# Performance work log

Measured on AMD Instinct MI355X. Metric: run time of the kernel, lower is better.

## Reference

```python
import jax, jax.numpy as jnp
import numpy as np

N, E, C, L, R, H = 10000, 100000, 64, 9, 9, 8
HD = C // H
F0 = 64          # radial feature dim (fc_neurons[0])
WN = R * C       # CP tensor-product weight numel


def _silu(x):
    return x * jax.nn.sigmoid(x)


def _smooth_lrelu(x, a=0.2):
    return (1 + a) / 2 * x + (1 - a) / 2 * x * (2 * jax.nn.sigmoid(x) - 1)


def _lin(x, W, b=None):
    # equivariant Linear over channel dim; bias applied only to scalar (l=0) component
    y = jnp.einsum('elc,cd->eld', x, W)
    if b is not None:
        y = y.at[:, 0, :].add(b)
    return y


def _cp_tp(x, sh, w, U, V, Y):
    # CP-decomposed SH tensor product:
    # out[e,m,c] = sum_r U[m,r] * (sum_m1 V[m1,r] x[e,m1,c]) * (sum_m2 Y[m2,r] sh[e,m2]) * w[e,r,c]
    xv = jnp.einsum('elc,lr->erc', x, V)          # [E,R,C]
    ys = jnp.einsum('el,lr->er', sh, Y)           # [E,R]
    return jnp.einsum('erc,lr->elc', xv * ys[:, :, None] * w, U)


def setup_inputs():
    key = jax.random.key(0)
    ks = jax.random.split(key, 32)
    f32 = jnp.float32
    s = 1.0 / np.sqrt(C)
    return {
        'node_input': jax.random.normal(ks[0], (N, L, C), f32),
        'edge_attr': jax.random.normal(ks[1], (E, L), f32),
        'edge_scalars': jax.random.normal(ks[2], (E, F0), f32),
        'W_src': jax.random.normal(ks[3], (C, C), f32) * s,
        'b_src': jnp.zeros((C,), f32),
        'W_dst': jax.random.normal(ks[4], (C, C), f32) * s,
        'rad_w1': jax.random.normal(ks[5], (F0, F0), f32) / np.sqrt(F0),
        'rad_b1': jnp.zeros((F0,), f32),
        'rad_ln_w': jnp.ones((F0,), f32),
        'rad_ln_b': jnp.zeros((F0,), f32),
        'rad_w2': jax.random.normal(ks[6], (F0, WN), f32) / np.sqrt(F0),
        'rad_offset': jax.random.uniform(ks[7], (WN,), f32, -1.0 / np.sqrt(F0), 1.0 / np.sqrt(F0)),
        'U1': jax.random.normal(ks[8], (L, R), f32) / np.sqrt(R),
        'V1': jax.random.normal(ks[9], (L, R), f32) / np.sqrt(L),
        'Y1': jax.random.normal(ks[10], (L, R), f32) / np.sqrt(L),
        'U2': jax.random.normal(ks[11], (L, R), f32) / np.sqrt(R),
        'V2': jax.random.normal(ks[12], (L, R), f32) / np.sqrt(L),
        'Y2': jax.random.normal(ks[13], (L, R), f32) / np.sqrt(L),
        'W_alpha': jax.random.normal(ks[14], (C, C), f32) * s,
        'b_alpha': jnp.zeros((C,), f32),
        'alpha_dot': jax.random.normal(ks[15], (H, HD), f32) / np.sqrt(HD),
        'W_value': jax.random.normal(ks[16], (C, 2 * C), f32) * s,
        'b_value': jnp.zeros((2 * C,), f32),
        'W_proj': jax.random.normal(ks[17], (C, C), f32) * s,
        'b_proj': jnp.zeros((C,), f32),
        'edge_src': jax.random.randint(ks[18], (E,), 0, N),
        'edge_dst': jax.random.randint(ks[19], (E,), 0, N),
    }


def reference(node_input, edge_attr, edge_scalars, W_src, b_src, W_dst,
              rad_w1, rad_b1, rad_ln_w, rad_ln_b, rad_w2, rad_offset,
              U1, V1, Y1, U2, V2, Y2, W_alpha, b_alpha, alpha_dot,
              W_value, b_value, W_proj, b_proj, edge_src, edge_dst):
    n = node_input.shape[0]
    # per-edge message: gather of src/dst projected features
    msg = _lin(node_input, W_src, b_src)[edge_src] + _lin(node_input, W_dst)[edge_dst]
    # RadialProfile MLP -> CP tensor-product weights [E,R,C]
    h = edge_scalars @ rad_w1 + rad_b1
    h = (h - h.mean(-1, keepdims=True)) / jnp.sqrt(h.var(-1, keepdims=True) + 1e-5)
    h = _silu(h * rad_ln_w + rad_ln_b)
    w = (h @ rad_w2 + rad_offset).reshape(-1, R, C)
    msg = _cp_tp(msg, edge_attr, w, U1, V1, Y1)
    # attention logits from scalar (0e) channel
    a = _lin(msg, W_alpha, b_alpha)[:, 0, :].reshape(-1, H, HD)
    a = jnp.einsum('ekd,kd->ek', _smooth_lrelu(a), alpha_dot)
    # segment softmax over destination nodes
    amax = jax.ops.segment_max(a, edge_dst, num_segments=n)
    a = jnp.exp(a - amax[edge_dst])
    asum = jax.ops.segment_sum(a, edge_dst, num_segments=n)
    a = a / (asum[edge_dst] + 1e-16)  # dropout = identity at eval
    # value path: gated nonlinearity, second CP tensor product
    v = _lin(msg, W_value, b_value)
    val, gate = v[..., :C], jax.nn.sigmoid(v[:, 0, C:])[:, None, :]
    v = jnp.concatenate([_silu(val[:, :1, :]), val[:, 1:, :] * gate], axis=1)
    v = _cp_tp(v, edge_attr, w, U2, V2, Y2)
    v = v.reshape(-1, L, H, HD) * a[:, None, :, None]
    out = jax.ops.segment_sum(v, edge_dst, num_segments=n).reshape(n, L, C)
    return _lin(out, W_proj, b_proj)
```

## Files before the change

kernel.cpp:

```cpp
#include <hip/hip_runtime.h>
#include <hip/hip_bf16.h>

#define NN 10000
#define EE 100000
#define LL 9
#define HH 8
#define NLC (NN*LL*64)

typedef float f32x4 __attribute__((ext_vector_type(4)));
typedef short bf16x8 __attribute__((ext_vector_type(8)));
typedef unsigned short u16x4 __attribute__((ext_vector_type(4)));

__device__ __forceinline__ float sigmoidf_(float x){ return 1.0f/(1.0f+__expf(-x)); }
__device__ __forceinline__ unsigned short f2bf(float x){
  __hip_bfloat16 b = __float2bfloat16(x);
  return *reinterpret_cast<unsigned short*>(&b);
}
__device__ __forceinline__ float bf2f(unsigned short b){ return __uint_as_float(((unsigned)b)<<16); }

__device__ __forceinline__ bf16x8 ldA(const unsigned short* plane, int ln, int kt){
  const int row = ln & 15;
  const int col = (kt*32 + ((ln>>4)<<3)) ^ ((row & 7) << 3);
  return *(const bf16x8*)(plane + row*64 + col);
}

__global__ __launch_bounds__(256) void k_prep_mat(
    const float* __restrict__ W, int ncol,
    unsigned short* __restrict__ bh, unsigned short* __restrict__ bl)
{
  const int t = blockIdx.x*256 + threadIdx.x;
  if (t >= (ncol>>4)*1024) return;
  const int i  = t & 7;
  const int ln = (t >> 3) & 63;
  const int kt = (t >> 9) & 1;
  const int nt = t >> 10;
  const int k  = kt*32 + ((ln>>4)<<3) + i;
  const int col = nt*16 + (ln & 15);
  const float v = W[k*ncol + col];
  const unsigned short h = f2bf(v);
  bh[t] = h;
  bl[t] = f2bf(v - bf2f(h));
}

__global__ __launch_bounds__(256) void k_prep_vab(
    const float* __restrict__ Wv, const float* __restrict__ Wa,
    unsigned short* __restrict__ bh, unsigned short* __restrict__ bl)
{
  const int t = blockIdx.x*256 + threadIdx.x;
  if (t >= 12*1024) return;
  const int i  = t & 7;
  const int ln = (t >> 3) & 63;
  const int kt = (t >> 9) & 1;
  const int nt = t >> 10;
  const int k  = kt*32 + ((ln>>4)<<3) + i;
  const int col = nt*16 + (ln & 15);
  const float v = (col < 128) ? Wv[k*128 + col] : Wa[k*64 + (col - 128)];
  const unsigned short h = f2bf(v);
  bh[t] = h;
  bl[t] = f2bf(v - bf2f(h));
}

__global__ __launch_bounds__(256) void k_node_lin_mfma(
    const float* __restrict__ x, const float* __restrict__ bs,
    const unsigned short* __restrict__ wsdh, const unsigned short* __restrict__ wsdl,
    float* __restrict__ xs, float* __restrict__ xd)
{
  const int tid = threadIdx.x, wid = tid>>6, ln = tid&63;
  const int base = blockIdx.x * 16;
  __shared__ unsigned short hx[2][16][64];
  {
    const int row = tid >> 4, c4 = (tid & 15) * 4;
    const float4 v = *(const float4*)&x[(size_t)(base+row)*64 + c4];
    const int cs = c4 ^ ((row & 7) << 3);
    u16x4 h, l;
    h[0]=f2bf(v.x); h[1]=f2bf(v.y); h[2]=f2bf(v.z); h[3]=f2bf(v.w);
    l[0]=f2bf(v.x-bf2f(h[0])); l[1]=f2bf(v.y-bf2f(h[1]));
    l[2]=f2bf(v.z-bf2f(h[2])); l[3]=f2bf(v.w-bf2f(h[3]));
    *(u16x4*)&hx[0][row][cs] = h;
    *(u16x4*)&hx[1][row][cs] = l;
  }
  __syncthreads();
  const bf16x8 ah0 = ldA(&hx[0][0][0], ln, 0);
  const bf16x8 ah1 = ldA(&hx[0][0][0], ln, 1);
  const bf16x8 al0 = ldA(&hx[1][0][0], ln, 0);
  const bf16x8 al1 = ldA(&hx[1][0][0], ln, 1);
  const bf16x8* Bh = (const bf16x8*)wsdh;
  const bf16x8* Bl = (const bf16x8*)wsdl;
  const int col = wid*16 + (ln & 15);
  const int r0  = (ln >> 4) * 4;
  #pragma unroll
  for (int g = 0; g < 2; g++){
    const int nt = g*4 + wid;
    f32x4 d = {0.f,0.f,0.f,0.f};
    const bf16x8 bh0 = Bh[(nt*2+0)*64 + ln];
    const bf16x8 bl0 = Bl[(nt*2+0)*64 + ln];
    const bf16x8 bh1 = Bh[(nt*2+1)*64 + ln];
    const bf16x8 bl1 = Bl[(nt*2+1)*64 + ln];
    d = __builtin_amdgcn_mfma_f32_16x16x32_bf16(ah0, bh0, d, 0, 0, 0);
    d = __builtin_amdgcn_mfma_f32_16x16x32_bf16(al0, bh0, d, 0, 0, 0);
    d = __builtin_amdgcn_mfma_f32_16x16x32_bf16(ah0, bl0, d, 0, 0, 0);
    d = __builtin_amdgcn_mfma_f32_16x16x32_bf16(ah1, bh1, d, 0, 0, 0);
    d = __builtin_amdgcn_mfma_f32_16x16x32_bf16(al1, bh1, d, 0, 0, 0);
    d = __builtin_amdgcn_mfma_f32_16x16x32_bf16(ah1, bl1, d, 0, 0, 0);
    float* out = (g == 0) ? xs : xd;
    #pragma unroll
    for (int i = 0; i < 4; i++){
      const int row = base + r0 + i;
      float o = d[i];
      if (g == 0 && row % LL == 0) o += bs[col];
      out[(size_t)row*64 + col] = o;
    }
  }
}

__global__ __launch_bounds__(512, 4) void k_edge_fused(
    const float* __restrict__ xsrc, const float* __restrict__ xdst,
    const float* __restrict__ eattr, const float* __restrict__ escal,
    const float* __restrict__ w1, const float* __restrict__ b1,
    const float* __restrict__ lnw, const float* __restrict__ lnb,
    const float* __restrict__ woff,
    const float* __restrict__ U1, const float* __restrict__ V1, const float* __restrict__ Y1,
    const float* __restrict__ U2, const float* __restrict__ V2, const float* __restrict__ Y2,
    const float* __restrict__ ba, const float* __restrict__ adot,
    const float* __restrict__ bv,
    const unsigned short* __restrict__ w2h, const unsigned short* __restrict__ w2l,
    const unsigned short* __restrict__ vabh, const unsigned short* __restrict__ vabl,
    const int* __restrict__ esrc, const int* __restrict__ edst,
    float* __restrict__ accum, float* __restrict__ asum)
{
  const int tid = threadIdx.x;
  const int wid = tid >> 6;
  const int ln  = tid & 63;
  const int base = blockIdx.x * 16;

  __shared__ float sgse[2][16][64];
  __shared__ unsigned short wle[16][576];
  __shared__ unsigned short ms2[9][16][64];
  __shared__ float sU1[9][12], sV1[9][12], sU2[9][12], sV2[9][12];
  __shared__ float syv1[16][12], syv2[16][12];
  float (*se)[64] = sgse[0];
  unsigned short* hpl = (unsigned short*)&sgse[1][0][0];

  for (int i = tid; i < 81; i += 512){
    const int r9 = i/9, c9 = i%9;
    sU1[r9][c9]=U1[i]; sV1[r9][c9]=V1[i]; sU2[r9][c9]=U2[i]; sV2[r9][c9]=V2[i];
  }
  if (tid < 144){
    const int er = tid/9, r = tid%9;
    const float* ea = eattr + (size_t)(base+er)*9;
    float y1 = 0.f, y2 = 0.f;
    #pragma unroll
    for (int l = 0; l < 9; l++){ y1 += ea[l]*Y1[l*9+r]; y2 += ea[l]*Y2[l*9+r]; }
    syv1[er][r] = y1; syv2[er][r] = y2;
  }
  for (int i = tid; i < 1024; i += 512) se[i>>6][i&63] = escal[(size_t)base*64 + i];
  __syncthreads();

  {
    const int c = ln;
    const float bb = b1[c];
    float hv_[2] = {bb, bb};
    for (int kq = 0; kq < 16; kq++){
      const int k0 = kq*4;
      const float a0 = w1[(k0+0)*64+c], a1 = w1[(k0+1)*64+c], a2 = w1[(k0+2)*64+c], a3 = w1[(k0+3)*64+c];
      #pragma unroll
      for (int j = 0; j < 2; j++){
        const float4 xv = *(const float4*)&se[wid*2+j][k0];
        hv_[j] += xv.x*a0 + xv.y*a1 + xv.z*a2 + xv.w*a3;
      }
    }
    const float lw = lnw[c], lb = lnb[c];
    #pragma unroll
    for (int j = 0; j < 2; j++){
      const float v = hv_[j];
      float s1 = v, s2 = v*v;
      #pragma unroll
      for (int m = 1; m < 64; m <<= 1){ s1 += __shfl_xor(s1, m, 64); s2 += __shfl_xor(s2, m, 64); }
      const float mean = s1 * (1.0f/64.0f);
      const float var  = s2 * (1.0f/64.0f) - mean*mean;
      const float g = (v - mean) * rsqrtf(var + 1e-5f) * lw + lb;
      const float hj = g * sigmoidf_(g);
      const int er = wid*2 + j;
      const int cs = c ^ ((er & 7) << 3);
      const unsigned short hb = f2bf(hj);
      hpl[(0*16 + er)*64 + cs] = hb;
      hpl[(1*16 + er)*64 + cs] = f2bf(hj - bf2f(hb));
    }
  }
  __syncthreads();

  {
    const bf16x8 ah0 = ldA(hpl, ln, 0);
    const bf16x8 ah1 = ldA(hpl, ln, 1);
    const bf16x8 al0 = ldA(hpl + 16*64, ln, 0);
    const bf16x8 al1 = ldA(hpl + 16*64, ln, 1);
    const bf16x8* Bh = (const bf16x8*)w2h;
    const bf16x8* Bl = (const bf16x8*)w2l;
    const int q = ln >> 4, p = ln & 15;
    #pragma unroll
    for (int t5 = 0; t5 < 5; t5++){
      const int nt = wid + 8*t5;
      if (nt < 36){
        f32x4 d = {0.f,0.f,0.f,0.f};
        const bf16x8 bh0 = Bh[(nt*2+0)*64 + ln];
        const bf16x8 bl0 = Bl[(nt*2+0)*64 + ln];
        const bf16x8 bh1 = Bh[(nt*2+1)*64 + ln];
        const bf16x8 bl1 = Bl[(nt*2+1)*64 + ln];
        d = __builtin_amdgcn_mfma_f32_16x16x32_bf16(ah0, bh0, d, 0, 0, 0);
        d = __builtin_amdgcn_mfma_f32_16x16x32_bf16(al0, bh0, d, 0, 0, 0);
        d = __builtin_amdgcn_mfma_f32_16x16x32_bf16(ah0, bl0, d, 0, 0, 0);
        d = __builtin_amdgcn_mfma_f32_16x16x32_bf16(ah1, bh1, d, 0, 0, 0);
        d = __builtin_amdgcn_mfma_f32_16x16x32_bf16(al1, bh1, d, 0, 0, 0);
        d = __builtin_amdgcn_mfma_f32_16x16x32_bf16(ah1, bl1, d, 0, 0, 0);
        const int col = nt*16 + p;
        const float wo = woff[col];
        #pragma unroll
        for (int i = 0; i < 4; i++) wle[q*4+i][col] = f2bf(d[i] + wo);
      }
    }
  }
  __syncthreads();

  {
    const int c = ln;
    const int er0 = wid*2;
    float msg[2][9];
    #pragma unroll
    for (int j = 0; j < 2; j++){
      const int e  = base + er0 + j;
      const int src = esrc[e], dst = edst[e];
      const float* ps = xsrc + (size_t)src*576 + c;
      const float* pd = xdst + (size_t)dst*576 + c;
      #pragma unroll
      for (int l = 0; l < 9; l++) msg[j][l] = ps[l*64] + pd[l*64];
    }
    float xv[2][9];
    #pragma unroll
    for (int j = 0; j < 2; j++)
      #pragma unroll
      for (int r = 0; r < 9; r++) xv[j][r] = 0.f;
    #pragma unroll
    for (int l = 0; l < 9; l++){
      const float4 v0 = *(const float4*)&sV1[l][0];
      const float4 v1 = *(const float4*)&sV1[l][4];
      const float  v2 = sV1[l][8];
      #pragma unroll
      for (int j = 0; j < 2; j++){
        const float m = msg[j][l];
        xv[j][0] += m*v0.x; xv[j][1] += m*v0.y; xv[j][2] += m*v0.z; xv[j][3] += m*v0.w;
        xv[j][4] += m*v1.x; xv[j][5] += m*v1.y; xv[j][6] += m*v1.z; xv[j][7] += m*v1.w;
        xv[j][8] += m*v2;
      }
    }
    #pragma unroll
    for (int j = 0; j < 2; j++){
      const int er = er0 + j;
      const float4 s0 = *(const float4*)&syv1[er][0];
      const float4 s1 = *(const float4*)&syv1[er][4];
      const float  s2 = syv1[er][8];
      const float sy[9] = {s0.x,s0.y,s0.z,s0.w,s1.x,s1.y,s1.z,s1.w,s2};
      #pragma unroll
      for (int r = 0; r < 9; r++) xv[j][r] *= sy[r] * bf2f(wle[er][r*64+c]);
    }
    #pragma unroll
    for (int l = 0; l < 9; l++){
      const float4 u0 = *(const float4*)&sU1[l][0];
      const float4 u1 = *(const float4*)&sU1[l][4];
      const float  u2 = sU1[l][8];
      #pragma unroll
      for (int j = 0; j < 2; j++){
        const int er = er0 + j;
        const float m2 = xv[j][0]*u0.x + xv[j][1]*u0.y + xv[j][2]*u0.z + xv[j][3]*u0.w
                       + xv[j][4]*u1.x + xv[j][5]*u1.y + xv[j][6]*u1.z + xv[j][7]*u1.w
                       + xv[j][8]*u2;
        ms2[l][er][c ^ ((er & 7) << 3)] = f2bf(m2);
      }
    }
  }
  __syncthreads();

  f32x4 vacc[9];
  {
    const bf16x8* Bh = (const bf16x8*)vabh;
    const bf16x8* Bl = (const bf16x8*)vabl;
    if (wid < 4){
      const int nt = wid;
      const bf16x8 bh0 = Bh[(nt*2+0)*64 + ln];
      const bf16x8 bl0 = Bl[(nt*2+0)*64 + ln];
      const bf16x8 bh1 = Bh[(nt*2+1)*64 + ln];
      const bf16x8 bl1 = Bl[(nt*2+1)*64 + ln];
      #pragma unroll
      for (int l = 0; l < 9; l++){
        const bf16x8 a0 = ldA(&ms2[l][0][0], ln, 0);
        const bf16x8 a1 = ldA(&ms2[l][0][0], ln, 1);
        f32x4 d = {0.f,0.f,0.f,0.f};
        d = __builtin_amdgcn_mfma_f32_16x16x32_bf16(a0, bh0, d, 0, 0, 0);
        d = __builtin_amdgcn_mfma_f32_16x16x32_bf16(a0, bl0, d, 0, 0, 0);
        d = __builtin_amdgcn_mfma_f32_16x16x32_bf16(a1, bh1, d, 0, 0, 0);
        d = __builtin_amdgcn_mfma_f32_16x16x32_bf16(a1, bl1, d, 0, 0, 0);
        vacc[l] = d;
      }
    } else {
      const int w4 = wid - 4;
      const bf16x8 a0 = ldA(&ms2[0][0][0], ln, 0);
      const bf16x8 a1 = ldA(&ms2[0][0][0], ln, 1);
      const int q = ln >> 4, p = ln & 15;
      #pragma unroll
      for (int gg = 0; gg < 2; gg++){
        const int nt = 4 + gg*4 + w4;
        const bf16x8 bh0 = Bh[(nt*2+0)*64 + ln];
        const bf16x8 bl0 = Bl[(nt*2+0)*64 + ln];
        const bf16x8 bh1 = Bh[(nt*2+1)*64 + ln];
        const bf16x8 bl1 = Bl[(nt*2+1)*64 + ln];
        f32x4 d = {0.f,0.f,0.f,0.f};
        d = __builtin_amdgcn_mfma_f32_16x16x32_bf16(a0, bh0, d, 0, 0, 0);
        d = __builtin_amdgcn_mfma_f32_16x16x32_bf16(a0, bl0, d, 0, 0, 0);
        d = __builtin_amdgcn_mfma_f32_16x16x32_bf16(a1, bh1, d, 0, 0, 0);
        d = __builtin_amdgcn_mfma_f32_16x16x32_bf16(a1, bl1, d, 0, 0, 0);
        #pragma unroll
        for (int i = 0; i < 4; i++) sgse[gg][q*4+i][w4*16+p] = d[i];
      }
    }
  }
  __syncthreads();

  if (wid < 4){
    const int col = wid*16 + (ln & 15);
    const int r0  = (ln >> 4) * 4;
    #pragma unroll
    for (int l = 0; l < 9; l++)
      #pragma unroll
      for (int i = 0; i < 4; i++){
        const int er = r0 + i;
        ms2[l][er][col ^ ((er & 7) << 3)] = f2bf(vacc[l][i]);
      }
  }
  __syncthreads();

  {
    const int c = ln;
    const int er0 = wid*2;
    const float bvc = bv[c], bgc = bv[64+c], bac = ba[c], adc = adot[c];
    int dsti[2]; float gsv[2], pev[2];
    #pragma unroll
    for (int j = 0; j < 2; j++){
      const int er = er0 + j;
      dsti[j] = edst[base + er];
      gsv[j] = sigmoidf_(sgse[0][er][c] + bgc);
      const float a  = sgse[1][er][c] + bac;
      const float sl = 0.2f*a + 0.8f*a*sigmoidf_(a);
      float t = sl * adc;
      t += __shfl_xor(t, 1, 64);
      t += __shfl_xor(t, 2, 64);
      t += __shfl_xor(t, 4, 64);
      pev[j] = __expf(t);
      if ((c & 7) == 0) atomicAdd(&asum[(size_t)dsti[j]*8 + (c>>3)], pev[j]);
    }
    float tmp2[2][9];
    #pragma unroll
    for (int j = 0; j < 2; j++)
      #pragma unroll
      for (int r = 0; r < 9; r++) tmp2[j][r] = 0.f;
    #pragma unroll
    for (int l = 0; l < 9; l++){
      const float4 v0 = *(const float4*)&sV2[l][0];
      const float4 v1 = *(const float4*)&sV2[l][4];
      const float  v2 = sV2[l][8];
      #pragma unroll
      for (int j = 0; j < 2; j++){
        const int er = er0 + j;
        float v = bf2f(ms2[l][er][c ^ ((er & 7) << 3)]);
        if (l == 0){ v += bvc; v = v * sigmoidf_(v); }
        else v *= gsv[j];
        tmp2[j][0] += v*v0.x; tmp2[j][1] += v*v0.y; tmp2[j][2] += v*v0.z; tmp2[j][3] += v*v0.w;
        tmp2[j][4] += v*v1.x; tmp2[j][5] += v*v1.y; tmp2[j][6] += v*v1.z; tmp2[j][7] += v*v1.w;
        tmp2[j][8] += v*v2;
      }
    }
    #pragma unroll
    for (int j = 0; j < 2; j++){
      const int er = er0 + j;
      const float4 s0 = *(const float4*)&syv2[er][0];
      const float4 s1 = *(const float4*)&syv2[er][4];
      const float  s2 = syv2[er][8];
      const float sy[9] = {s0.x,s0.y,s0.z,s0.w,s1.x,s1.y,s1.z,s1.w,s2};
      #pragma unroll
      for (int r = 0; r < 9; r++) tmp2[j][r] *= sy[r] * bf2f(wle[er][r*64+c]) * pev[j];
    }
    #pragma unroll
    for (int l = 0; l < 9; l++){
      const float4 u0 = *(const float4*)&sU2[l][0];
      const float4 u1 = *(const float4*)&sU2[l][4];
      const float  u2 = sU2[l][8];
      #pragma unroll
      for (int j = 0; j < 2; j++){
        const float o = tmp2[j][0]*u0.x + tmp2[j][1]*u0.y + tmp2[j][2]*u0.z + tmp2[j][3]*u0.w
                      + tmp2[j][4]*u1.x + tmp2[j][5]*u1.y + tmp2[j][6]*u1.z + tmp2[j][7]*u1.w
                      + tmp2[j][8]*u2;
        atomicAdd(accum + (size_t)dsti[j]*576 + l*64 + c, o);
      }
    }
  }
}

__global__ __launch_bounds__(256) void k_norm_proj_mfma(
    const float* __restrict__ acc, const float* __restrict__ asum,
    const unsigned short* __restrict__ wph, const unsigned short* __restrict__ wpl,
    const float* __restrict__ bp, float* __restrict__ out)
{
  const int tid = threadIdx.x, wid = tid>>6, ln = tid&63;
  const int base = blockIdx.x * 16;
  __shared__ unsigned short hx[2][16][64];
  {
    const int row = tid >> 4, c4 = (tid & 15) * 4;
    const int grow = base + row;
    const float s = 1.0f / (asum[(size_t)(grow/9)*8 + (c4>>3)] + 1e-16f);
    float4 v = *(const float4*)&acc[(size_t)grow*64 + c4];
    v.x *= s; v.y *= s; v.z *= s; v.w *= s;
    const int cs = c4 ^ ((row & 7) << 3);
    u16x4 h, l;
    h[0]=f2bf(v.x); h[1]=f2bf(v.y); h[2]=f2bf(v.z); h[3]=f2bf(v.w);
    l[0]=f2bf(v.x-bf2f(h[0])); l[1]=f2bf(v.y-bf2f(h[1]));
    l[2]=f2bf(v.z-bf2f(h[2])); l[3]=f2bf(v.w-bf2f(h[3]));
    *(u16x4*)&hx[0][row][cs] = h;
    *(u16x4*)&hx[1][row][cs] = l;
  }
  __syncthreads();
  const bf16x8 ah0 = ldA(&hx[0][0][0], ln, 0);
  const bf16x8 ah1 = ldA(&hx[0][0][0], ln, 1);
  const bf16x8 al0 = ldA(&hx[1][0][0], ln, 0);
  const bf16x8 al1 = ldA(&hx[1][0][0], ln, 1);
  const bf16x8* Bh = (const bf16x8*)wph;
  const bf16x8* Bl = (const bf16x8*)wpl;
  const int nt = wid;
  f32x4 d = {0.f,0.f,0.f,0.f};
  const bf16x8 bh0 = Bh[(nt*2+0)*64 + ln];
  const bf16x8 bl0 = Bl[(nt*2+0)*64 + ln];
  const bf16x8 bh1 = Bh[(nt*2+1)*64 + ln];
  const bf16x8 bl1 = Bl[(nt*2+1)*64 + ln];
  d = __builtin_amdgcn_mfma_f32_16x16x32_bf16(ah0, bh0, d, 0, 0, 0);
  d = __builtin_amdgcn_mfma_f32_16x16x32_bf16(al0, bh0, d, 0, 0, 0);
  d = __builtin_amdgcn_mfma_f32_16x16x32_bf16(ah0, bl0, d, 0, 0, 0);
  d = __builtin_amdgcn_mfma_f32_16x16x32_bf16(ah1, bh1, d, 0, 0, 0);
  d = __builtin_amdgcn_mfma_f32_16x16x32_bf16(al1, bh1, d, 0, 0, 0);
  d = __builtin_amdgcn_mfma_f32_16x16x32_bf16(ah1, bl1, d, 0, 0, 0);
  const int col = wid*16 + (ln & 15);
  const int r0  = (ln >> 4) * 4;
  #pragma unroll
  for (int i = 0; i < 4; i++){
    const int row = base + r0 + i;
    float o = d[i];
    if (row % LL == 0) o += bp[col];
    out[(size_t)row*64 + col] = o;
  }
}

extern "C" void kernel_launch(void* const* d_in, const int* in_sizes, int n_in,
                              void* d_out, int out_size, void* d_ws, size_t ws_size,
                              hipStream_t stream)
{
  (void)in_sizes; (void)n_in; (void)out_size;
  const float* node_input = (const float*)d_in[0];
  const float* edge_attr  = (const float*)d_in[1];
  const float* edge_scal  = (const float*)d_in[2];
  const float* W_src   = (const float*)d_in[3];
  const float* b_src   = (const float*)d_in[4];
  const float* W_dst   = (const float*)d_in[5];
  const float* rad_w1  = (const float*)d_in[6];
  const float* rad_b1  = (const float*)d_in[7];
  const float* rad_ln_w= (const float*)d_in[8];
  const float* rad_ln_b= (const float*)d_in[9];
  const float* rad_w2  = (const float*)d_in[10];
  const float* rad_off = (const float*)d_in[11];
  const float* U1 = (const float*)d_in[12];
  const float* V1 = (const float*)d_in[13];
  const float* Y1 = (const float*)d_in[14];
  const float* U2 = (const float*)d_in[15];
  const float* V2 = (const float*)d_in[16];
  const float* Y2 = (const float*)d_in[17];
  const float* W_alpha = (const float*)d_in[18];
  const float* b_alpha = (const float*)d_in[19];
  const float* alpha_dot = (const float*)d_in[20];
  const float* W_value = (const float*)d_in[21];
  const float* b_value = (const float*)d_in[22];
  const float* W_proj  = (const float*)d_in[23];
  const float* b_proj  = (const float*)d_in[24];
  const int* esrc = (const int*)d_in[25];
  const int* edst = (const int*)d_in[26];

  float* xsrc  = (float*)d_ws;
  float* xdst  = xsrc + NLC;
  float* accum = xdst + NLC;
  float* asum  = accum + NLC;
  unsigned short* w2h  = (unsigned short*)(asum + (size_t)NN*HH);
  unsigned short* w2l  = w2h + 36*1024;
  unsigned short* vabh = w2l + 36*1024;
  unsigned short* vabl = vabh + 12*1024;
  unsigned short* wsdh = vabl + 12*1024;
  unsigned short* wsdl = wsdh + 8*1024;
  unsigned short* wph  = wsdl + 8*1024;
  unsigned short* wpl  = wph  + 4*1024;
  const size_t need = ((size_t)3*NLC + (size_t)NN*HH)*sizeof(float)
                    + (size_t)(2*36*1024 + 2*12*1024 + 2*8*1024 + 2*4*1024)*sizeof(unsigned short);
  if (ws_size < need) return;

  hipMemsetAsync(accum, 0, (size_t)NLC*sizeof(float), stream);
  hipMemsetAsync(asum, 0, (size_t)NN*HH*sizeof(float), stream);

  k_prep_mat<<<144, 256, 0, stream>>>(rad_w2, 576, w2h, w2l);
  k_prep_vab<<<48, 256, 0, stream>>>(W_value, W_alpha, vabh, vabl);
  k_prep_mat<<<16, 256, 0, stream>>>(W_src, 64, wsdh, wsdl);
  k_prep_mat<<<16, 256, 0, stream>>>(W_dst, 64, wsdh + 4*1024, wsdl + 4*1024);
  k_prep_mat<<<16, 256, 0, stream>>>(W_proj, 64, wph, wpl);
  k_node_lin_mfma<<<NN*LL/16, 256, 0, stream>>>(node_input, b_src, wsdh, wsdl, xsrc, xdst);
  k_edge_fused<<<EE/16, 512, 0, stream>>>(xsrc, xdst, edge_attr, edge_scal,
      rad_w1, rad_b1, rad_ln_w, rad_ln_b, rad_off,
      U1, V1, Y1, U2, V2, Y2,
      b_alpha, alpha_dot, b_value,
      w2h, w2l, vabh, vabl, esrc, edst, accum, asum);
  k_norm_proj_mfma<<<NN*LL/16, 256, 0, stream>>>(accum, asum, wph, wpl, b_proj, (float*)d_out);
}
```

Before: 291.3 us.

## Split fused edge kernel into radial-weight producer and edge consumer kernels

The monolithic edge kernel is split into two kernels. The first computes the radial MLP and its per-edge weights [E,576] and stores them as bf16 in workspace. The second does the gather, both CP tensor products, attention and scatter using those weights, processing edges in chunks sized to the available workspace. This is meant to lower per-kernel register and LDS pressure and raise occupancy, at the cost of a round trip to global memory for roughly 115 MB of weights and reduced weight precision. It falls back to the fused kernel when workspace is insufficient.

```diff
diff --git a/kernel.cpp b/kernel.cpp
--- a/kernel.cpp
+++ b/kernel.cpp
@@ -109,6 +109,309 @@
       float o = d[i];
       if (g == 0 && row % LL == 0) o += bs[col];
       out[(size_t)row*64 + col] = o;
+    }
+  }
+}
+
+
+__global__ __launch_bounds__(512, 4) void k_radial_w2(
+    const float* __restrict__ escal,
+    const float* __restrict__ w1, const float* __restrict__ b1,
+    const float* __restrict__ lnw, const float* __restrict__ lnb,
+    const float* __restrict__ woff,
+    const unsigned short* __restrict__ w2h, const unsigned short* __restrict__ w2l,
+    int e0, unsigned short* __restrict__ wbuf)
+{
+  const int tid = threadIdx.x, wid = tid>>6, ln = tid&63;
+  const int lbase = blockIdx.x * 16;
+  const int base  = e0 + lbase;
+  __shared__ float se[16][64];
+  __shared__ unsigned short hpl[2][16][64];
+
+  for (int i = tid; i < 1024; i += 512) se[i>>6][i&63] = escal[(size_t)base*64 + i];
+  __syncthreads();
+
+  {
+    const int c = ln;
+    const float bb = b1[c];
+    float hv_[2] = {bb, bb};
+    for (int kq = 0; kq < 16; kq++){
+      const int k0 = kq*4;
+      const float a0 = w1[(k0+0)*64+c], a1 = w1[(k0+1)*64+c], a2 = w1[(k0+2)*64+c], a3 = w1[(k0+3)*64+c];
+      #pragma unroll
+      for (int j = 0; j < 2; j++){
+        const float4 xv = *(const float4*)&se[wid*2+j][k0];
+        hv_[j] += xv.x*a0 + xv.y*a1 + xv.z*a2 + xv.w*a3;
+      }
+    }
+    const float lw = lnw[c], lb = lnb[c];
+    #pragma unroll
+    for (int j = 0; j < 2; j++){
+      const float v = hv_[j];
+      float s1 = v, s2 = v*v;
+      #pragma unroll
+      for (int m = 1; m < 64; m <<= 1){ s1 += __shfl_xor(s1, m, 64); s2 += __shfl_xor(s2, m, 64); }
+      const float mean = s1 * (1.0f/64.0f);
+      const float var  = s2 * (1.0f/64.0f) - mean*mean;
+      const float g = (v - mean) * rsqrtf(var + 1e-5f) * lw + lb;
+      const float hj = g * sigmoidf_(g);
+      const int er = wid*2 + j;
+      const int cs = c ^ ((er & 7) << 3);
+      const unsigned short hb = f2bf(hj);
+      hpl[0][er][cs] = hb;
+      hpl[1][er][cs] = f2bf(hj - bf2f(hb));
+    }
+  }
+  __syncthreads();
+
+  {
+    const bf16x8 ah0 = ldA(&hpl[0][0][0], ln, 0);
+    const bf16x8 ah1 = ldA(&hpl[0][0][0], ln, 1);
+    const bf16x8 al0 = ldA(&hpl[1][0][0], ln, 0);
+    const bf16x8 al1 = ldA(&hpl[1][0][0], ln, 1);
+    const bf16x8* Bh = (const bf16x8*)w2h;
+    const bf16x8* Bl = (const bf16x8*)w2l;
+    const int q = ln >> 4, p = ln & 15;
+    #pragma unroll
+    for (int t5 = 0; t5 < 5; t5++){
+      const int nt = wid + 8*t5;
+      if (nt < 36){
+        f32x4 d = {0.f,0.f,0.f,0.f};
+        const bf16x8 bh0 = Bh[(nt*2+0)*64 + ln];
+        const bf16x8 bl0 = Bl[(nt*2+0)*64 + ln];
+        const bf16x8 bh1 = Bh[(nt*2+1)*64 + ln];
+        const bf16x8 bl1 = Bl[(nt*2+1)*64 + ln];
+        d = __builtin_amdgcn_mfma_f32_16x16x32_bf16(ah0, bh0, d, 0, 0, 0);
+        d = __builtin_amdgcn_mfma_f32_16x16x32_bf16(al0, bh0, d, 0, 0, 0);
+        d = __builtin_amdgcn_mfma_f32_16x16x32_bf16(ah0, bl0, d, 0, 0, 0);
+        d = __builtin_amdgcn_mfma_f32_16x16x32_bf16(ah1, bh1, d, 0, 0, 0);
+        d = __builtin_amdgcn_mfma_f32_16x16x32_bf16(al1, bh1, d, 0, 0, 0);
+        d = __builtin_amdgcn_mfma_f32_16x16x32_bf16(ah1, bl1, d, 0, 0, 0);
+        const int col = nt*16 + p;
+        const float wo = woff[col];
+        #pragma unroll
+        for (int i = 0; i < 4; i++)
+          wbuf[(size_t)(lbase + q*4 + i)*576 + col] = f2bf(d[i] + wo);
+      }
+    }
+  }
+}
+
+__global__ __launch_bounds__(512, 4) void k_edge_consume(
+    const float* __restrict__ xsrc, const float* __restrict__ xdst,
+    const float* __restrict__ eattr,
+    const float* __restrict__ U1, const float* __restrict__ V1, const float* __restrict__ Y1,
+    const float* __restrict__ U2, const float* __restrict__ V2, const float* __restrict__ Y2,
+    const float* __restrict__ ba, const float* __restrict__ adot,
+    const float* __restrict__ bv,
+    const unsigned short* __restrict__ vabh, const unsigned short* __restrict__ vabl,
+    const unsigned short* __restrict__ wbuf, int e0,
+    const int* __restrict__ esrc, const int* __restrict__ edst,
+    float* __restrict__ accum, float* __restrict__ asum)
+{
+  const int tid = threadIdx.x, wid = tid>>6, ln = tid&63;
+  const int lbase = blockIdx.x * 16;
+  const int base  = e0 + lbase;
+
+  __shared__ unsigned short ms2[9][16][64];
+  __shared__ float sga[2][16][64];
+  __shared__ float sU1[9][12], sV1[9][12], sU2[9][12], sV2[9][12];
+  __shared__ float syv1[16][12], syv2[16][12];
+
+  for (int i = tid; i < 81; i += 512){
+    const int r9 = i/9, c9 = i%9;
+    sU1[r9][c9]=U1[i]; sV1[r9][c9]=V1[i]; sU2[r9][c9]=U2[i]; sV2[r9][c9]=V2[i];
+  }
+  if (tid < 144){
+    const int er = tid/9, r = tid%9;
+    const float* ea = eattr + (size_t)(base+er)*9;
+    float y1 = 0.f, y2 = 0.f;
+    #pragma unroll
+    for (int l = 0; l < 9; l++){ y1 += ea[l]*Y1[l*9+r]; y2 += ea[l]*Y2[l*9+r]; }
+    syv1[er][r] = y1; syv2[er][r] = y2;
+  }
+  __syncthreads();
+
+  {
+    const int c = ln;
+    const int er0 = wid*2;
+    float msg[2][9];
+    #pragma unroll
+    for (int j = 0; j < 2; j++){
+      const int e  = base + er0 + j;
+      const int src = esrc[e], dst = edst[e];
+      const float* ps = xsrc + (size_t)src*576 + c;
+      const float* pd = xdst + (size_t)dst*576 + c;
+      #pragma unroll
+      for (int l = 0; l < 9; l++) msg[j][l] = ps[l*64] + pd[l*64];
+    }
+    float xv[2][9];
+    #pragma unroll
+    for (int j = 0; j < 2; j++)
+      #pragma unroll
+      for (int r = 0; r < 9; r++) xv[j][r] = 0.f;
+    #pragma unroll
+    for (int l = 0; l < 9; l++){
+      const float4 v0 = *(const float4*)&sV1[l][0];
+      const float4 v1 = *(const float4*)&sV1[l][4];
+      const float  v2 = sV1[l][8];
+      #pragma unroll
+      for (int j = 0; j < 2; j++){
+        const float m = msg[j][l];
+        xv[j][0] += m*v0.x; xv[j][1] += m*v0.y; xv[j][2] += m*v0.z; xv[j][3] += m*v0.w;
+        xv[j][4] += m*v1.x; xv[j][5] += m*v1.y; xv[j][6] += m*v1.z; xv[j][7] += m*v1.w;
+        xv[j][8] += m*v2;
+      }
+    }
+    #pragma unroll
+    for (int j = 0; j < 2; j++){
+      const int er = er0 + j;
+      const unsigned short* wb = wbuf + (size_t)(lbase + er)*576 + c;
+      const float4 s0 = *(const float4*)&syv1[er][0];
+      const float4 s1 = *(const float4*)&syv1[er][4];
+      const float  s2 = syv1[er][8];
+      const float sy[9] = {s0.x,s0.y,s0.z,s0.w,s1.x,s1.y,s1.z,s1.w,s2};
+      #pragma unroll
+      for (int r = 0; r < 9; r++) xv[j][r] *= sy[r] * bf2f(wb[r*64]);
+    }
+    #pragma unroll
+    for (int l = 0; l < 9; l++){
+      const float4 u0 = *(const float4*)&sU1[l][0];
+      const float4 u1 = *(const float4*)&sU1[l][4];
+      const float  u2 = sU1[l][8];
+      #pragma unroll
+      for (int j = 0; j < 2; j++){
+        const int er = er0 + j;
+        const float m2 = xv[j][0]*u0.x + xv[j][1]*u0.y + xv[j][2]*u0.z + xv[j][3]*u0.w
+                       + xv[j][4]*u1.x + xv[j][5]*u1.y + xv[j][6]*u1.z + xv[j][7]*u1.w
+                       + xv[j][8]*u2;
+        ms2[l][er][c ^ ((er & 7) << 3)] = f2bf(m2);
+      }
+    }
+  }
+  __syncthreads();
+
+  f32x4 vacc[9];
+  {
+    const bf16x8* Bh = (const bf16x8*)vabh;
+    const bf16x8* Bl = (const bf16x8*)vabl;
+    if (wid < 4){
+      const int nt = wid;
+      const bf16x8 bh0 = Bh[(nt*2+0)*64 + ln];
+      const bf16x8 bl0 = Bl[(nt*2+0)*64 + ln];
+      const bf16x8 bh1 = Bh[(nt*2+1)*64 + ln];
+      const bf16x8 bl1 = Bl[(nt*2+1)*64 + ln];
+      #pragma unroll
+      for (int l = 0; l < 9; l++){
+        const bf16x8 a0 = ldA(&ms2[l][0][0], ln, 0);
+        const bf16x8 a1 = ldA(&ms2[l][0][0], ln, 1);
+        f32x4 d = {0.f,0.f,0.f,0.f};
+        d = __builtin_amdgcn_mfma_f32_16x16x32_bf16(a0, bh0, d, 0, 0, 0);
+        d = __builtin_amdgcn_mfma_f32_16x16x32_bf16(a0, bl0, d, 0, 0, 0);
+        d = __builtin_amdgcn_mfma_f32_16x16x32_bf16(a1, bh1, d, 0, 0, 0);
+        d = __builtin_amdgcn_mfma_f32_16x16x32_bf16(a1, bl1, d, 0, 0, 0);
+        vacc[l] = d;
+      }
+    } else {
+      const int w4 = wid - 4;
+      const bf16x8 a0 = ldA(&ms2[0][0][0], ln, 0);
+      const bf16x8 a1 = ldA(&ms2[0][0][0], ln, 1);
+      const int q = ln >> 4, p = ln & 15;
+      #pragma unroll
+      for (int gg = 0; gg < 2; gg++){
+        const int nt = 4 + gg*4 + w4;
+        const bf16x8 bh0 = Bh[(nt*2+0)*64 + ln];
+        const bf16x8 bl0 = Bl[(nt*2+0)*64 + ln];
+        const bf16x8 bh1 = Bh[(nt*2+1)*64 + ln];
+        const bf16x8 bl1 = Bl[(nt*2+1)*64 + ln];
+        f32x4 d = {0.f,0.f,0.f,0.f};
+        d = __builtin_amdgcn_mfma_f32_16x16x32_bf16(a0, bh0, d, 0, 0, 0);
+        d = __builtin_amdgcn_mfma_f32_16x16x32_bf16(a0, bl0, d, 0, 0, 0);
+        d = __builtin_amdgcn_mfma_f32_16x16x32_bf16(a1, bh1, d, 0, 0, 0);
+        d = __builtin_amdgcn_mfma_f32_16x16x32_bf16(a1, bl1, d, 0, 0, 0);
+        #pragma unroll
+        for (int i = 0; i < 4; i++) sga[gg][q*4+i][w4*16+p] = d[i];
+      }
+    }
+  }
+  __syncthreads();
+
+  if (wid < 4){
+    const int col = wid*16 + (ln & 15);
+    const int r0  = (ln >> 4) * 4;
+    #pragma unroll
+    for (int l = 0; l < 9; l++)
+      #pragma unroll
+      for (int i = 0; i < 4; i++){
+        const int er = r0 + i;
+        ms2[l][er][col ^ ((er & 7) << 3)] = f2bf(vacc[l][i]);
+      }
+  }
+  __syncthreads();
+
+  {
+    const int c = ln;
+    const int er0 = wid*2;
+    const float bvc = bv[c], bgc = bv[64+c], bac = ba[c], adc = adot[c];
+    int dsti[2]; float gsv[2], pev[2];
+    #pragma unroll
+    for (int j = 0; j < 2; j++){
+      const int er = er0 + j;
+      dsti[j] = edst[base + er];
+      gsv[j] = sigmoidf_(sga[0][er][c] + bgc);
+      const float a  = sga[1][er][c] + bac;
+      const float sl = 0.2f*a + 0.8f*a*sigmoidf_(a);
+      float t = sl * adc;
+      t += __shfl_xor(t, 1, 64);
+      t += __shfl_xor(t, 2, 64);
+      t += __shfl_xor(t, 4, 64);
+      pev[j] = __expf(t);
+      if ((c & 7) == 0) atomicAdd(&asum[(size_t)dsti[j]*8 + (c>>3)], pev[j]);
+    }
+    float tmp2[2][9];
+    #pragma unroll
+    for (int j = 0; j < 2; j++)
+      #pragma unroll
+      for (int r = 0; r < 9; r++) tmp2[j][r] = 0.f;
+    #pragma unroll
+    for (int l = 0; l < 9; l++){
+      const float4 v0 = *(const float4*)&sV2[l][0];
+      const float4 v1 = *(const float4*)&sV2[l][4];
+      const float  v2 = sV2[l][8];
+      #pragma unroll
+      for (int j = 0; j < 2; j++){
+        const int er = er0 + j;
+        float v = bf2f(ms2[l][er][c ^ ((er & 7) << 3)]);
+        if (l == 0){ v += bvc; v = v * sigmoidf_(v); }
+        else v *= gsv[j];
+        tmp2[j][0] += v*v0.x; tmp2[j][1] += v*v0.y; tmp2[j][2] += v*v0.z; tmp2[j][3] += v*v0.w;
+        tmp2[j][4] += v*v1.x; tmp2[j][5] += v*v1.y; tmp2[j][6] += v*v1.z; tmp2[j][7] += v*v1.w;
+        tmp2[j][8] += v*v2;
+      }
+    }
+    #pragma unroll
+    for (int j = 0; j < 2; j++){
+      const int er = er0 + j;
+      const unsigned short* wb = wbuf + (size_t)(lbase + er)*576 + c;
+      const float4 s0 = *(const float4*)&syv2[er][0];
+      const float4 s1 = *(const float4*)&syv2[er][4];
+      const float  s2 = syv2[er][8];
+      const float sy[9] = {s0.x,s0.y,s0.z,s0.w,s1.x,s1.y,s1.z,s1.w,s2};
+      #pragma unroll
+      for (int r = 0; r < 9; r++) tmp2[j][r] *= sy[r] * bf2f(wb[r*64]) * pev[j];
+    }
+    #pragma unroll
+    for (int l = 0; l < 9; l++){
+      const float4 u0 = *(const float4*)&sU2[l][0];
+      const float4 u1 = *(const float4*)&sU2[l][4];
+      const float  u2 = sU2[l][8];
+      #pragma unroll
+      for (int j = 0; j < 2; j++){
+        const float o = tmp2[j][0]*u0.x + tmp2[j][1]*u0.y + tmp2[j][2]*u0.z + tmp2[j][3]*u0.w
+                      + tmp2[j][4]*u1.x + tmp2[j][5]*u1.y + tmp2[j][6]*u1.z + tmp2[j][7]*u1.w
+                      + tmp2[j][8]*u2;
+        atomicAdd(accum + (size_t)dsti[j]*576 + l*64 + c, o);
+      }
     }
   }
 }
@@ -500,9 +803,16 @@
   unsigned short* wsdl = wsdh + 8*1024;
   unsigned short* wph  = wsdl + 8*1024;
   unsigned short* wpl  = wph  + 4*1024;
-  const size_t need = ((size_t)3*NLC + (size_t)NN*HH)*sizeof(float)
-                    + (size_t)(2*36*1024 + 2*12*1024 + 2*8*1024 + 2*4*1024)*sizeof(unsigned short);
-  if (ws_size < need) return;
+  unsigned short* wbuf = wpl  + 4*1024;
+  const size_t base_need = ((size_t)3*NLC + (size_t)NN*HH)*sizeof(float)
+                         + (size_t)(2*36*1024 + 2*12*1024 + 2*8*1024 + 2*4*1024)*sizeof(unsigned short);
+  if (ws_size < base_need) return;
+
+  int CS = 0;
+  const int cands[4] = {100000, 50000, 20000, 10000};
+  for (int i = 0; i < 4; i++){
+    if (base_need + (size_t)cands[i]*576*sizeof(unsigned short) <= ws_size){ CS = cands[i]; break; }
+  }
 
   hipMemsetAsync(accum, 0, (size_t)NLC*sizeof(float), stream);
   hipMemsetAsync(asum, 0, (size_t)NN*HH*sizeof(float), stream);
@@ -513,10 +823,23 @@
   k_prep_mat<<<16, 256, 0, stream>>>(W_dst, 64, wsdh + 4*1024, wsdl + 4*1024);
   k_prep_mat<<<16, 256, 0, stream>>>(W_proj, 64, wph, wpl);
   k_node_lin_mfma<<<NN*LL/16, 256, 0, stream>>>(node_input, b_src, wsdh, wsdl, xsrc, xdst);
-  k_edge_fused<<<EE/16, 512, 0, stream>>>(xsrc, xdst, edge_attr, edge_scal,
-      rad_w1, rad_b1, rad_ln_w, rad_ln_b, rad_off,
-      U1, V1, Y1, U2, V2, Y2,
-      b_alpha, alpha_dot, b_value,
-      w2h, w2l, vabh, vabl, esrc, edst, accum, asum);
+
+  if (CS > 0){
+    for (int e0 = 0; e0 < EE; e0 += CS){
+      const int n = (EE - e0 < CS) ? (EE - e0) : CS;
+      k_radial_w2<<<n/16, 512, 0, stream>>>(edge_scal, rad_w1, rad_b1, rad_ln_w, rad_ln_b,
+          rad_off, w2h, w2l, e0, wbuf);
+      k_edge_consume<<<n/16, 512, 0, stream>>>(xsrc, xdst, edge_attr,
+          U1, V1, Y1, U2, V2, Y2, b_alpha, alpha_dot, b_value,
+          vabh, vabl, wbuf, e0, esrc, edst, accum, asum);
+    }
+  } else {
+    k_edge_fused<<<EE/16, 512, 0, stream>>>(xsrc, xdst, edge_attr, edge_scal,
+        rad_w1, rad_b1, rad_ln_w, rad_ln_b, rad_off,
+        U1, V1, Y1, U2, V2, Y2,
+        b_alpha, alpha_dot, b_value,
+        w2h, w2l, vabh, vabl, esrc, edst, accum, asum);
+  }
+
   k_norm_proj_mfma<<<NN*LL/16, 256, 0, stream>>>(accum, asum, wph, wpl, b_proj, (float*)d_out);
 }
```

Result: slower. 341.0 us (+17.1%).
